# Optimization experiments

Hardware: AMD Instinct MI355X
Metric: run time of the kernel (lower is better)

Reference implementation:

```python
import jax, jax.numpy as jnp
import numpy as np

NUM_GRIDS = 16
IN_X, IN_Z, OUT, BATCH = 32, 32, 64, 512


def _borders_cdf_grid(n_chunks):
    def inv_cdf(u):
        return np.log(2.0 * u) if u <= 0.5 else -np.log(2.0 * (1.0 - u))
    cs = 1.0 / n_chunks
    b = [inv_cdf(i * cs) for i in range(1, n_chunks)]
    left = b[0] - (b[1] - b[0])
    right = b[-1] + (b[-1] - b[-2])
    return np.array([left] + b + [right], dtype=np.float32)


def _laplace_cdf(v):
    e = jnp.exp(-jnp.abs(v))
    return jnp.where(v > 0, 1.0 - 0.5 * e, 0.5 * e)


def setup_inputs() -> dict:
    key = jax.random.key(0)
    k1, k2, k3 = jax.random.split(key, 3)
    scale = 0.1 / np.sqrt(IN_X * IN_Z)
    borders_np = _borders_cdf_grid(NUM_GRIDS)
    inv_len_np = (1.0 / (borders_np[1:] - borders_np[:-1])).astype(np.float32)
    return {
        "x": jax.random.normal(k1, (IN_X, BATCH), dtype=jnp.float32),
        "z": jax.random.normal(k2, (IN_Z, BATCH), dtype=jnp.float32),
        "func_parameter": jax.random.uniform(
            k3, (NUM_GRIDS + 1, NUM_GRIDS + 1, OUT, IN_X, IN_Z),
            dtype=jnp.float32, minval=-scale, maxval=scale),
        "borders": jnp.asarray(borders_np),
        "inverse_chunk_lengths": jnp.asarray(inv_len_np[:NUM_GRIDS]),
    }


def reference(x, z, func_parameter, borders, inverse_chunk_lengths):
    G = inverse_chunk_lengths.shape[0]
    Ix, B = x.shape
    Iz = z.shape[0]

    # data-dependent bin indices per (input_dim, batch) element
    idx_x = jnp.clip((_laplace_cdf(x) * G).astype(jnp.int32), 0, G - 1)  # [Ix,B]
    idx_z = jnp.clip((_laplace_cdf(z) * G).astype(jnp.int32), 0, G - 1)  # [Iz,B]
    dx = (x - borders[idx_x]) * inverse_chunk_lengths[idx_x]             # [Ix,B]
    dz = (z - borders[idx_z]) * inverse_chunk_lengths[idx_z]             # [Iz,B]
    idx_xn = jnp.clip(idx_x + 1, 0, G)
    idx_zn = jnp.clip(idx_z + 1, 0, G)

    # [Ix, Iz, G+1, G+1, O] so the per-(ix,iz) tables are leading-indexed
    Pt = jnp.transpose(func_parameter, (3, 4, 0, 1, 2))
    ax = jnp.arange(Ix)[:, None, None]   # [Ix,1,1]
    az = jnp.arange(Iz)[None, :, None]   # [1,Iz,1]

    def corner(ii, jj):  # ii:[Ix,1,B] or broadcastable, jj:[1,Iz,B]
        return Pt[ax, az, ii, jj]        # -> [Ix,Iz,B,O]

    ixb, ixnb = idx_x[:, None, :], idx_xn[:, None, :]
    izb, iznb = idx_z[None, :, :], idx_zn[None, :, :]
    wx, wz = dx[:, None, :], dz[None, :, :]             # [Ix,1,B],[1,Iz,B]

    out = (
        jnp.einsum('xzb,xzbo->ob', (1 - wx) * (1 - wz), corner(ixb, izb))
        + jnp.einsum('xzb,xzbo->ob', (1 - wx) * wz, corner(ixb, iznb))
        + jnp.einsum('xzb,xzbo->ob', wx * (1 - wz), corner(ixnb, izb))
        + jnp.einsum('xzb,xzbo->ob', wx * wz, corner(ixnb, iznb))
    )
    return out  # [output_dim, batch]
```

## Files before the change

### kernel.cpp

```cpp
#include <hip/hip_runtime.h>
#include <hip/hip_fp16.h>


#define NG        16
#define NB        17
#define IN_X      32
#define IN_Z      32
#define OUT_DIM   64
#define BATCH     512
#define CELLS     (NB * NB)
#define CSTRIDE   133
#define ILSTRIDE  33
#define XSTR_A    (NB * CSTRIDE)
#define STASKS    (CELLS * 32)

typedef __fp16 h2v __attribute__((ext_vector_type(2)));

__device__ __forceinline__ unsigned pack_h2(float a, float b) {
    h2v v = __builtin_amdgcn_cvt_pkrtz(a, b);
    return __builtin_bit_cast(unsigned, v);
}
__device__ __forceinline__ __half2 u2h(unsigned u) {
    return __builtin_bit_cast(__half2, u);
}

__device__ __forceinline__ void grid_coord(float v,
                                           const float* __restrict__ borders,
                                           const float* __restrict__ inv_len,
                                           int& idx, float& w) {
    float e   = expf(-fabsf(v));
    float cdf = (v > 0.f) ? (1.f - 0.5f * e) : (0.5f * e);
    int t = (int)(cdf * 16.f);
    t = t < 0 ? 0 : (t > NG - 1 ? NG - 1 : t);
    idx = t;
    w = (v - borders[t]) * inv_len[t];
}

__global__ __launch_bounds__(1024, 4)
void bf2d_fused(const float* __restrict__ x,
                const float* __restrict__ z,
                const float* __restrict__ borders,
                const float* __restrict__ inv_len,
                const float* __restrict__ P,
                float* __restrict__ out) {
    __shared__ unsigned lds[CELLS * CSTRIDE];

    const int tid = threadIdx.x;
    const int op  = blockIdx.x & 31;
    const int iq  = blockIdx.x >> 5;
    const int o0  = op * 2;
    const int b   = tid & (BATCH - 1);
    const int ih  = tid >> 9;
    const int il0 = 2 * ih, il1 = 2 * ih + 1;

    const float* Pb = P + (size_t)o0 * 1024 + iq * 128;

    float4 a0v, b0v;
    {
        const int c = tid >> 5, f4 = tid & 31;
        const float* g = Pb + (size_t)c * 65536 + f4 * 4;
        a0v = *(const float4*)g;
        b0v = *(const float4*)(g + 1024);
    }

    unsigned ztab[IN_Z];
    #pragma unroll
    for (int j = 0; j < IN_Z; ++j) {
        int idx; float w;
        grid_coord(z[j * BATCH + b], borders, inv_len, idx, w);
        ztab[j] = ((unsigned)(idx * CSTRIDE) << 16)
                | (pack_h2(w, 0.f) & 0xFFFFu);
    }
    int xi0, xi1; float xw0f, xw1f;
    grid_coord(x[(iq * 4 + il0) * BATCH + b], borders, inv_len, xi0, xw0f);
    grid_coord(x[(iq * 4 + il1) * BATCH + b], borders, inv_len, xi1, xw1f);
    const __half2 wx0 = u2h(pack_h2(xw0f, xw0f));
    const __half2 wx1 = u2h(pack_h2(xw1f, xw1f));
    const int xo0 = xi0 * XSTR_A + il0 * ILSTRIDE;
    const int xo1 = xi1 * XSTR_A + il1 * ILSTRIDE;

    {
        const int c = tid >> 5, f4 = tid & 31;
        unsigned* d = &lds[c * CSTRIDE + (f4 >> 3) * ILSTRIDE
                           + ((f4 & 7) << 2)];
        d[0] = pack_h2(a0v.x, b0v.x);
        d[1] = pack_h2(a0v.y, b0v.y);
        d[2] = pack_h2(a0v.z, b0v.z);
        d[3] = pack_h2(a0v.w, b0v.w);
    }
    #pragma unroll
    for (int it = 1; it < 10; ++it) {
        const int k = tid + it * 1024;
        if (k < STASKS) {
            const int c  = k >> 5;
            const int f4 = k & 31;
            const float* g = Pb + (size_t)c * 65536 + f4 * 4;
            const float4 a = *(const float4*)g;
            const float4 bb = *(const float4*)(g + 1024);
            unsigned* d = &lds[c * CSTRIDE + (f4 >> 3) * ILSTRIDE
                               + ((f4 & 7) << 2)];
            d[0] = pack_h2(a.x, bb.x);
            d[1] = pack_h2(a.y, bb.y);
            d[2] = pack_h2(a.z, bb.z);
            d[3] = pack_h2(a.w, bb.w);
        }
    }
    __syncthreads();

    __half2 acc0 = __float2half2_rn(0.f);
    __half2 acc1 = __float2half2_rn(0.f);
    #pragma unroll
    for (int j = 0; j < IN_Z; ++j) {
        const unsigned u  = ztab[j];
        const unsigned lo = u & 0xFFFFu;
        const __half2 wz  = u2h(lo | (lo << 16));
        const int     zo  = (int)(u >> 16) + j;
        {
            const int base = xo0 + zo;
            const __half2 q0 = u2h(lds[base]);
            const __half2 q1 = u2h(lds[base + CSTRIDE]);
            const __half2 v0 = u2h(lds[base + XSTR_A]);
            const __half2 v1 = u2h(lds[base + XSTR_A + CSTRIDE]);
            const __half2 zlo = __hfma2(wz, __hsub2(q1, q0), q0);
            const __half2 zhi = __hfma2(wz, __hsub2(v1, v0), v0);
            acc0 = __hadd2(acc0, __hfma2(wx0, __hsub2(zhi, zlo), zlo));
        }
        {
            const int base = xo1 + zo;
            const __half2 q0 = u2h(lds[base]);
            const __half2 q1 = u2h(lds[base + CSTRIDE]);
            const __half2 v0 = u2h(lds[base + XSTR_A]);
            const __half2 v1 = u2h(lds[base + XSTR_A + CSTRIDE]);
            const __half2 zlo = __hfma2(wz, __hsub2(q1, q0), q0);
            const __half2 zhi = __hfma2(wz, __hsub2(v1, v0), v0);
            acc1 = __hadd2(acc1, __hfma2(wx1, __hsub2(zhi, zlo), zlo));
        }
    }

    const float accx = __low2float(acc0)  + __low2float(acc1);
    const float accy = __high2float(acc0) + __high2float(acc1);

    atomicAdd(&out[o0 * BATCH + b],       accx);
    atomicAdd(&out[(o0 + 1) * BATCH + b], accy);
}

extern "C" void kernel_launch(void* const* d_in, const int* in_sizes, int n_in,
                              void* d_out, int out_size, void* d_ws, size_t ws_size,
                              hipStream_t stream) {
    const float* x       = (const float*)d_in[0];
    const float* z       = (const float*)d_in[1];
    const float* P       = (const float*)d_in[2];
    const float* borders = (const float*)d_in[3];
    const float* inv_len = (const float*)d_in[4];
    float* out = (float*)d_out;

    hipMemsetAsync(out, 0, OUT_DIM * BATCH * sizeof(float), stream);
    bf2d_fused<<<dim3(32 * 8), dim3(1024), 0, stream>>>(
        x, z, borders, inv_len, P, out);
}
```

Measured before the change: 141.5 us.

## Compute z grid coords inside main loop and stage borders tables in LDS

Removes the 32-entry per-thread ztab register array and instead computes each z bin index and weight on the fly inside the accumulation loop, with the borders and inverse-length tables staged in shared memory. The P staging loop now runs in one uniform loop after the table load, and x coordinates are computed after the barrier. The launch-bounds occupancy hint is dropped. This cuts register pressure, but the exp and global z loads move into the hot loop and are recomputed per thread, and they are no longer overlapped with the P loads before the barrier.

```diff
diff --git a/kernel.cpp b/kernel.cpp
--- a/kernel.cpp
+++ b/kernel.cpp
@@ -24,19 +24,18 @@
     return __builtin_bit_cast(__half2, u);
 }
 
-__device__ __forceinline__ void grid_coord(float v,
-                                           const float* __restrict__ borders,
-                                           const float* __restrict__ inv_len,
-                                           int& idx, float& w) {
+__device__ __forceinline__ void grid_coord_lds(float v,
+                                               const float* __restrict__ tabs,
+                                               int& idx, float& w) {
     float e   = expf(-fabsf(v));
     float cdf = (v > 0.f) ? (1.f - 0.5f * e) : (0.5f * e);
     int t = (int)(cdf * 16.f);
     t = t < 0 ? 0 : (t > NG - 1 ? NG - 1 : t);
     idx = t;
-    w = (v - borders[t]) * inv_len[t];
+    w = (v - tabs[t]) * tabs[NB + t];
 }
 
-__global__ __launch_bounds__(1024, 4)
+__global__ __launch_bounds__(1024)
 void bf2d_fused(const float* __restrict__ x,
                 const float* __restrict__ z,
                 const float* __restrict__ borders,
@@ -44,6 +43,7 @@
                 const float* __restrict__ P,
                 float* __restrict__ out) {
     __shared__ unsigned lds[CELLS * CSTRIDE];
+    __shared__ float tabs[NB + NG];
 
     const int tid = threadIdx.x;
     const int op  = blockIdx.x & 31;
@@ -53,43 +53,12 @@
     const int ih  = tid >> 9;
     const int il0 = 2 * ih, il1 = 2 * ih + 1;
 
+    if (tid < NB + NG)
+        tabs[tid] = (tid < NB) ? borders[tid] : inv_len[tid - NB];
+
     const float* Pb = P + (size_t)o0 * 1024 + iq * 128;
-
-    float4 a0v, b0v;
-    {
-        const int c = tid >> 5, f4 = tid & 31;
-        const float* g = Pb + (size_t)c * 65536 + f4 * 4;
-        a0v = *(const float4*)g;
-        b0v = *(const float4*)(g + 1024);
-    }
-
-    unsigned ztab[IN_Z];
     #pragma unroll
-    for (int j = 0; j < IN_Z; ++j) {
-        int idx; float w;
-        grid_coord(z[j * BATCH + b], borders, inv_len, idx, w);
-        ztab[j] = ((unsigned)(idx * CSTRIDE) << 16)
-                | (pack_h2(w, 0.f) & 0xFFFFu);
-    }
-    int xi0, xi1; float xw0f, xw1f;
-    grid_coord(x[(iq * 4 + il0) * BATCH + b], borders, inv_len, xi0, xw0f);
-    grid_coord(x[(iq * 4 + il1) * BATCH + b], borders, inv_len, xi1, xw1f);
-    const __half2 wx0 = u2h(pack_h2(xw0f, xw0f));
-    const __half2 wx1 = u2h(pack_h2(xw1f, xw1f));
-    const int xo0 = xi0 * XSTR_A + il0 * ILSTRIDE;
-    const int xo1 = xi1 * XSTR_A + il1 * ILSTRIDE;
-
-    {
-        const int c = tid >> 5, f4 = tid & 31;
-        unsigned* d = &lds[c * CSTRIDE + (f4 >> 3) * ILSTRIDE
-                           + ((f4 & 7) << 2)];
-        d[0] = pack_h2(a0v.x, b0v.x);
-        d[1] = pack_h2(a0v.y, b0v.y);
-        d[2] = pack_h2(a0v.z, b0v.z);
-        d[3] = pack_h2(a0v.w, b0v.w);
-    }
-    #pragma unroll
-    for (int it = 1; it < 10; ++it) {
+    for (int it = 0; it < 10; ++it) {
         const int k = tid + it * 1024;
         if (k < STASKS) {
             const int c  = k >> 5;
@@ -107,14 +76,24 @@
     }
     __syncthreads();
 
+    int xi0, xi1; float xw0f, xw1f;
+    grid_coord_lds(x[(iq * 4 + il0) * BATCH + b], tabs, xi0, xw0f);
+    grid_coord_lds(x[(iq * 4 + il1) * BATCH + b], tabs, xi1, xw1f);
+    const __half2 wx0 = u2h(pack_h2(xw0f, xw0f));
+    const __half2 wx1 = u2h(pack_h2(xw1f, xw1f));
+    const int xo0 = xi0 * XSTR_A + il0 * ILSTRIDE;
+    const int xo1 = xi1 * XSTR_A + il1 * ILSTRIDE;
+
+    const float* zp = z + b;
     __half2 acc0 = __float2half2_rn(0.f);
     __half2 acc1 = __float2half2_rn(0.f);
-    #pragma unroll
+    #pragma unroll 4
     for (int j = 0; j < IN_Z; ++j) {
-        const unsigned u  = ztab[j];
-        const unsigned lo = u & 0xFFFFu;
-        const __half2 wz  = u2h(lo | (lo << 16));
-        const int     zo  = (int)(u >> 16) + j;
+        int zi; float zwf;
+        grid_coord_lds(zp[j * BATCH], tabs, zi, zwf);
+        const unsigned wzu = pack_h2(zwf, zwf);
+        const __half2 wz = u2h(wzu);
+        const int zo = zi * CSTRIDE + j;
         {
             const int base = xo0 + zo;
             const __half2 q0 = u2h(lds[base]);
```

New measurement: 124.7 us. 1.14x faster.
